# Kernel tuning notes

Measured on AMD Instinct MI355X. Metric: run time of the kernel, lower is better.

The kernel has to match this reference:

```python
import jax, jax.numpy as jnp
import numpy as np

B, T, M, E = 2, 2048, 1024, 8
CAP = (2 * B * T) // E  # GShard top-2 capacity = 2*S/E = 1024


def setup_inputs() -> dict:
    key = jax.random.key(0)
    k1, k2, k3 = jax.random.split(key, 3)
    x = jax.random.normal(k1, (B, T, M), jnp.float32)
    wg = jax.random.normal(k2, (M, E), jnp.float32) * 0.02
    expert_w = jax.random.normal(k3, (E, M, M), jnp.float32) * 0.02
    expert_b = jnp.zeros((E, M), jnp.float32)
    return {"x": x, "wg": wg, "expert_w": expert_w, "expert_b": expert_b}


def _top2_gate(x2, wg, capacity):
    """fairseq/GShard Top2Gate (deterministic second-expert, no jitter).
    Returns (l_aux, combine_weights[S,E,C], dispatch_mask[S,E,C] bool)."""
    S = x2.shape[0]
    num_experts = wg.shape[1]
    logits = x2 @ wg                                  # [S, E]
    gates = jax.nn.softmax(logits, axis=-1)           # [S, E]
    # top-1 expert
    idx1 = jnp.argmax(gates, axis=1)
    mask1 = jax.nn.one_hot(idx1, num_experts, dtype=jnp.int32)
    # top-2 expert: argmax over logits with top-1 masked out
    neg_inf = jnp.finfo(logits.dtype).min
    logits_wo1 = jnp.where(mask1.astype(bool), neg_inf, logits)
    idx2 = jnp.argmax(logits_wo1, axis=1)
    mask2 = jax.nn.one_hot(idx2, num_experts, dtype=jnp.int32)
    # positions within each expert's buffer
    loc1 = jnp.cumsum(mask1, axis=0) - 1              # [S, E]
    loc2 = jnp.cumsum(mask2, axis=0) - 1 + jnp.sum(mask1, axis=0, keepdims=True)
    # load-balancing auxiliary loss
    me = jnp.mean(gates, axis=0)
    ce = jnp.mean(mask1.astype(gates.dtype), axis=0)
    l_aux = jnp.mean(me * ce) * (num_experts * num_experts)
    # drop tokens over capacity
    mask1 = mask1 * (loc1 < capacity).astype(jnp.int32)
    mask2 = mask2 * (loc2 < capacity).astype(jnp.int32)
    loc1_s = jnp.sum(loc1 * mask1, axis=1)            # [S]
    loc2_s = jnp.sum(loc2 * mask2, axis=1)
    m1f = mask1.astype(gates.dtype)
    m2f = mask2.astype(gates.dtype)
    gates1_s = jnp.sum(gates * m1f, axis=1)
    gates2_s = jnp.sum(gates * m2f, axis=1)
    denom = gates1_s + gates2_s
    denom = jnp.clip(denom, jnp.finfo(gates.dtype).eps, None)
    gates1 = gates1_s / denom
    gates2 = gates2_s / denom
    loc1_oh = jax.nn.one_hot(loc1_s, capacity, dtype=gates.dtype)  # [S, C]
    loc2_oh = jax.nn.one_hot(loc2_s, capacity, dtype=gates.dtype)
    combine1 = gates1[:, None, None] * m1f[:, :, None] * loc1_oh[:, None, :]
    combine2 = gates2[:, None, None] * m2f[:, :, None] * loc2_oh[:, None, :]
    combine_weights = combine1 + combine2             # [S, E, C]
    dispatch_mask = combine_weights > 0               # bool [S, E, C]
    return l_aux, combine_weights, dispatch_mask


def reference(x, wg, expert_w, expert_b):
    b, t, d = x.shape
    x2 = x.reshape(-1, d)                             # [S, M]
    l_aux, cw, dm = _top2_gate(x2, wg, CAP)
    dmf = dm.astype(x.dtype)                          # [S, E, C]
    # dispatch: (E*C, S) @ (S, M) -> per-expert token buffers [E, C, M]
    dispatched = jnp.einsum('sec,sm->ecm', dmf, x2)
    # per-expert Linear (single device: all experts local, all-to-all = identity)
    expert_out = jnp.einsum('ecm,emn->ecn', dispatched, expert_w) + expert_b[:, None, :]
    # combine: (S, E*C) @ (E*C, M) -> [S, M]
    combined = jnp.einsum('sec,ecm->sm', cw, expert_out)
    return combined.reshape(b, t, d), l_aux
```

## Files before the change

### kernel.cpp

```cpp
#include <hip/hip_runtime.h>

typedef unsigned short u16;
typedef unsigned int u32;
typedef unsigned long long u64;
typedef short v8s __attribute__((ext_vector_type(8)));
typedef float v4f __attribute__((ext_vector_type(4)));

#define S_TOK 4096
#define MDIM  1024
#define NEXP  8
#define CAPN  1024

__device__ __forceinline__ u16 f2bf(float f) {
  u32 u = __float_as_uint(f);
  u += 0x7FFFu + ((u >> 16) & 1u);
  return (u16)(u >> 16);
}
__device__ __forceinline__ float bf2f(u16 h) {
  return __uint_as_float(((u32)h) << 16);
}
__device__ __forceinline__ void gll16(const void* g, void* l) {
  __builtin_amdgcn_global_load_lds(
      (const __attribute__((address_space(1))) void*)g,
      (__attribute__((address_space(3))) void*)l, 16, 0, 0);
}

__global__ __launch_bounds__(256) void transw_kernel(const float* __restrict__ w,
                                                     u16* __restrict__ wT) {
  int b  = blockIdx.x;
  int e  = b >> 8;
  int mt = (b >> 4) & 15;
  int nt = b & 15;
  __shared__ float tile[64][65];
  const float* src = w + (size_t)e * MDIM * MDIM;
  u16* dst = wT + (size_t)e * MDIM * MDIM;
  int tid = threadIdx.x;
#pragma unroll
  for (int i = 0; i < 16; i++) {
    int idx = tid + i * 256;
    int r = idx >> 6, c = idx & 63;
    tile[r][c] = src[(size_t)(mt * 64 + r) * MDIM + nt * 64 + c];
  }
  __syncthreads();
#pragma unroll
  for (int i = 0; i < 16; i++) {
    int idx = tid + i * 256;
    int r = idx >> 6, c = idx & 63;
    dst[(size_t)(nt * 64 + r) * MDIM + mt * 64 + c] = f2bf(tile[c][r]);
  }
}

__global__ __launch_bounds__(256) void gate_kernel(const float* __restrict__ x,
                                                   const float* __restrict__ wg,
                                                   u16* __restrict__ xbf,
                                                   int4* __restrict__ grec,
                                                   float* __restrict__ gpart) {
  __shared__ float wls[NEXP * MDIM];
  __shared__ float gsh[4][NEXP];
  int tid = threadIdx.x;
  for (int i = tid; i < NEXP * MDIM; i += 256) {
    int m = i >> 3, e = i & 7;
    wls[e * MDIM + m] = wg[i];
  }
  __syncthreads();
  int wave = tid >> 6, lane = tid & 63;
  int s = blockIdx.x * 4 + wave;
  const float* xr = x + (size_t)s * MDIM;
  u16* xw = xbf + (size_t)s * MDIM;
  float acc[NEXP];
#pragma unroll
  for (int e = 0; e < NEXP; e++) acc[e] = 0.f;
#pragma unroll
  for (int j = 0; j < 16; j++) {
    int m = j * 64 + lane;
    float xv = xr[m];
    xw[m] = f2bf(xv);
#pragma unroll
    for (int e = 0; e < NEXP; e++) acc[e] = fmaf(xv, wls[e * MDIM + m], acc[e]);
  }
#pragma unroll
  for (int off = 32; off > 0; off >>= 1)
#pragma unroll
    for (int e = 0; e < NEXP; e++) acc[e] += __shfl_xor(acc[e], off, 64);

  if (lane == 0) {
    float mx = acc[0];
#pragma unroll
    for (int e = 1; e < NEXP; e++) mx = fmaxf(mx, acc[e]);
    float ex[NEXP], sum = 0.f;
#pragma unroll
    for (int e = 0; e < NEXP; e++) { ex[e] = expf(acc[e] - mx); sum += ex[e]; }
    float inv = 1.f / sum;
    int e1 = 0; float b1 = acc[0];
#pragma unroll
    for (int e = 1; e < NEXP; e++) if (acc[e] > b1) { b1 = acc[e]; e1 = e; }
    int e2 = -1; float b2 = -3.4e38f;
#pragma unroll
    for (int e = 0; e < NEXP; e++) if (e != e1 && acc[e] > b2) { b2 = acc[e]; e2 = e; }
    grec[s] = make_int4(e1, e2, __float_as_int(ex[e1] * inv), __float_as_int(ex[e2] * inv));
#pragma unroll
    for (int e = 0; e < NEXP; e++) gsh[wave][e] = ex[e] * inv;
  }
  __syncthreads();
  if (tid < NEXP)
    gpart[blockIdx.x * NEXP + tid] = gsh[0][tid] + gsh[1][tid] + gsh[2][tid] + gsh[3][tid];
}

__global__ __launch_bounds__(1024) void scan_kernel(const int4* __restrict__ grec,
                                                    int4* __restrict__ trec,
                                                    int* __restrict__ slot_token,
                                                    const float* __restrict__ gpart,
                                                    u16* __restrict__ zrow,
                                                    float* __restrict__ out) {
  __shared__ u64 wtot[16][4];
  __shared__ float gred[16][NEXP];
  int t = threadIdx.x, lane = t & 63, wave = t >> 6;

#pragma unroll
  for (int i = 0; i < 8; i++) slot_token[t + i * 1024] = -1;
  zrow[t] = 0;

  float4 p0 = ((const float4*)gpart)[t * 2];
  float4 p1 = ((const float4*)gpart)[t * 2 + 1];
  float gs[NEXP] = {p0.x, p0.y, p0.z, p0.w, p1.x, p1.y, p1.z, p1.w};
#pragma unroll
  for (int off = 32; off > 0; off >>= 1)
#pragma unroll
    for (int e = 0; e < NEXP; e++) gs[e] += __shfl_xor(gs[e], off, 64);
  if (lane == 0)
#pragma unroll
    for (int e = 0; e < NEXP; e++) gred[wave][e] = gs[e];

  int4 r[4];
#pragma unroll
  for (int i = 0; i < 4; i++) r[i] = grec[t * 4 + i];

  u64 a1 = 0, b1 = 0, a2 = 0, b2 = 0;
#pragma unroll
  for (int i = 0; i < 4; i++) {
    int x1 = r[i].x, x2 = r[i].y;
    if (x1 < 4) a1 += 1ULL << (x1 * 16); else b1 += 1ULL << ((x1 - 4) * 16);
    if (x2 < 4) a2 += 1ULL << (x2 * 16); else b2 += 1ULL << ((x2 - 4) * 16);
  }
  u64 ia1 = a1, ib1 = b1, ia2 = a2, ib2 = b2;
#pragma unroll
  for (int off = 1; off < 64; off <<= 1) {
    u64 s1 = __shfl_up(a1, off, 64), s2 = __shfl_up(b1, off, 64);
    u64 s3 = __shfl_up(a2, off, 64), s4 = __shfl_up(b2, off, 64);
    if (lane >= off) { a1 += s1; b1 += s2; a2 += s3; b2 += s4; }
  }
  if (lane == 63) { wtot[wave][0] = a1; wtot[wave][1] = b1; wtot[wave][2] = a2; wtot[wave][3] = b2; }
  __syncthreads();
  if (t < 16) {
    u64 v0 = wtot[t][0], v1 = wtot[t][1], v2 = wtot[t][2], v3 = wtot[t][3];
#pragma unroll
    for (int off = 1; off < 16; off <<= 1) {
      u64 s0 = __shfl_up(v0, off, 64), s1 = __shfl_up(v1, off, 64);
      u64 s2 = __shfl_up(v2, off, 64), s3 = __shfl_up(v3, off, 64);
      if (t >= off) { v0 += s0; v1 += s1; v2 += s2; v3 += s3; }
    }
    wtot[t][0] = v0; wtot[t][1] = v1; wtot[t][2] = v2; wtot[t][3] = v3;
  }
  __syncthreads();
  u64 o1 = 0, o2 = 0, o3 = 0, o4 = 0;
  if (wave > 0) { o1 = wtot[wave - 1][0]; o2 = wtot[wave - 1][1]; o3 = wtot[wave - 1][2]; o4 = wtot[wave - 1][3]; }
  u64 ea  = a1 + o1 - ia1;
  u64 eb  = b1 + o2 - ib1;
  u64 ea2 = a2 + o3 - ia2;
  u64 eb2 = b2 + o4 - ib2;
  u64 ta = wtot[15][0], tb = wtot[15][1];

  int base1[NEXP], base2[NEXP], cnt1[NEXP];
#pragma unroll
  for (int e = 0; e < 4; e++) {
    base1[e]     = (int)((ea  >> (e * 16)) & 0xFFFF);
    base1[4 + e] = (int)((eb  >> (e * 16)) & 0xFFFF);
    base2[e]     = (int)((ea2 >> (e * 16)) & 0xFFFF);
    base2[4 + e] = (int)((eb2 >> (e * 16)) & 0xFFFF);
    cnt1[e]      = (int)((ta  >> (e * 16)) & 0xFFFF);
    cnt1[4 + e]  = (int)((tb  >> (e * 16)) & 0xFFFF);
  }
#pragma unroll
  for (int i = 0; i < 4; i++) {
    int s = t * 4 + i;
    int e1 = r[i].x, e2 = r[i].y;
    float g1 = __int_as_float(r[i].z), g2 = __int_as_float(r[i].w);
    int l1 = 0, l2 = 0;
#pragma unroll
    for (int q = 0; q < NEXP; q++) {
      if (q == e1) { l1 = base1[q]; base1[q] = l1 + 1; }
      if (q == e2) { l2 = base2[q]; base2[q] = l2 + 1; }
    }
    int loc2 = l2 + cnt1[e2];
    bool k1 = l1 < CAPN;
    bool k2 = loc2 < CAPN;
    float g1s = k1 ? g1 : 0.f;
    float g2s = k2 ? g2 : 0.f;
    float denom = fmaxf(g1s + g2s, 1.1920929e-7f);
    float gn1 = g1s / denom, gn2 = g2s / denom;
    int slot1 = k1 ? e1 * CAPN + l1 : -1;
    int slot2 = k2 ? e2 * CAPN + loc2 : -1;
    trec[s] = make_int4(slot1, slot2, __float_as_int(gn1), __float_as_int(gn2));
    if (k1) slot_token[slot1] = s;
    if (k2) slot_token[slot2] = s;
  }
  if (t == 0) {
    float acc = 0.f;
#pragma unroll
    for (int e = 0; e < NEXP; e++) {
      float g = 0.f;
      for (int w = 0; w < 16; w++) g += gred[w][e];
      acc += g * (float)cnt1[e];
    }
    out[(size_t)S_TOK * MDIM] = 8.f * acc / (4096.f * 4096.f);
  }
}

__global__ __launch_bounds__(256, 2) void expert_gemm(const u16* __restrict__ xbf,
                                                      const u16* __restrict__ wT,
                                                      const int* __restrict__ slot_token,
                                                      const u16* __restrict__ zrow,
                                                      const float* __restrict__ bias,
                                                      u16* __restrict__ eoutb) {
  __shared__ __align__(16) u16 As[128 * 64];
  __shared__ __align__(16) u16 Bs[128 * 64];
  const int tid  = threadIdx.x;
  const int e    = blockIdx.x >> 6;
  const int tile = blockIdx.x & 63;
  const int tm   = (tile >> 3) << 7;
  const int tn   = (tile & 7) << 7;
  const int lane = tid & 63;
  const int wave = tid >> 6;
  const int wr = wave >> 1, wc = wave & 1;

  const u16* srcA[4];
  const u16* srcB[4];
#pragma unroll
  for (int it = 0; it < 4; ++it) {
    int off = tid * 16 + it * 4096;
    int row = off >> 7;
    int kb  = off & 127;
    int st  = slot_token[e * CAPN + tm + row];
    srcA[it] = (st >= 0 ? xbf + (size_t)st * MDIM : zrow) + (kb >> 1);
    srcB[it] = wT + (size_t)e * MDIM * MDIM + (size_t)(tn + row) * MDIM + (kb >> 1);
  }
  char* ldsA = (char*)As;
  char* ldsB = (char*)Bs;

  v4f acc[4][4];
#pragma unroll
  for (int i = 0; i < 4; i++)
#pragma unroll
    for (int j = 0; j < 4; j++) acc[i][j] = (v4f){0.f, 0.f, 0.f, 0.f};

  for (int k0 = 0; k0 < MDIM; k0 += 64) {
    __syncthreads();
#pragma unroll
    for (int it = 0; it < 4; ++it)
      gll16(srcA[it] + k0, ldsA + tid * 16 + it * 4096);
#pragma unroll
    for (int it = 0; it < 4; ++it)
      gll16(srcB[it] + k0, ldsB + tid * 16 + it * 4096);
    __syncthreads();

    const v8s* Ap = (const v8s*)As;
    const v8s* Bp = (const v8s*)Bs;
#pragma unroll
    for (int ks = 0; ks < 2; ++ks) {
      v8s af[4], bfr[4];
#pragma unroll
      for (int i = 0; i < 4; i++)
        af[i] = Ap[(wr * 64 + i * 16 + (lane & 15)) * 8 + ks * 4 + (lane >> 4)];
#pragma unroll
      for (int j = 0; j < 4; j++)
        bfr[j] = Bp[(wc * 64 + j * 16 + (lane & 15)) * 8 + ks * 4 + (lane >> 4)];
#pragma unroll
      for (int i = 0; i < 4; i++)
#pragma unroll
        for (int j = 0; j < 4; j++)
          acc[i][j] = __builtin_amdgcn_mfma_f32_16x16x32_bf16(af[i], bfr[j], acc[i][j], 0, 0, 0);
    }
  }

  const float* bp = bias + (size_t)e * MDIM;
  float bv[4];
#pragma unroll
  for (int j = 0; j < 4; j++) bv[j] = bp[tn + wc * 64 + j * 16 + (lane & 15)];
  u16* outp = eoutb + (size_t)e * CAPN * MDIM;
#pragma unroll
  for (int i = 0; i < 4; i++) {
#pragma unroll
    for (int rr = 0; rr < 4; rr++) {
      int row = tm + wr * 64 + i * 16 + (lane >> 4) * 4 + rr;
#pragma unroll
      for (int j = 0; j < 4; j++) {
        int col = tn + wc * 64 + j * 16 + (lane & 15);
        outp[(size_t)row * MDIM + col] = f2bf(acc[i][j][rr] + bv[j]);
      }
    }
  }
}

__global__ __launch_bounds__(256) void combine_kernel(const u16* __restrict__ eoutb,
                                                      const int4* __restrict__ trec,
                                                      float* __restrict__ out) {
  int s = blockIdx.x;
  int tid = threadIdx.x;
  int4 r = trec[s];
  float g1 = __int_as_float(r.z), g2 = __int_as_float(r.w);
  float4 res = make_float4(0.f, 0.f, 0.f, 0.f);
  if (r.x >= 0) {
    ushort4 o = ((const ushort4*)(eoutb + (size_t)r.x * MDIM))[tid];
    res.x += g1 * bf2f(o.x); res.y += g1 * bf2f(o.y);
    res.z += g1 * bf2f(o.z); res.w += g1 * bf2f(o.w);
  }
  if (r.y >= 0) {
    ushort4 o = ((const ushort4*)(eoutb + (size_t)r.y * MDIM))[tid];
    res.x += g2 * bf2f(o.x); res.y += g2 * bf2f(o.y);
    res.z += g2 * bf2f(o.z); res.w += g2 * bf2f(o.w);
  }
  ((float4*)out)[(size_t)s * 256 + tid] = res;
}

extern "C" void kernel_launch(void* const* d_in, const int* in_sizes, int n_in,
                              void* d_out, int out_size, void* d_ws, size_t ws_size,
                              hipStream_t stream) {
  (void)in_sizes; (void)n_in; (void)out_size; (void)ws_size;
  const float* x  = (const float*)d_in[0];
  const float* wg = (const float*)d_in[1];
  const float* ew = (const float*)d_in[2];
  const float* eb = (const float*)d_in[3];
  float* out = (float*)d_out;

  char* ws = (char*)d_ws;
  u16*   xbf   = (u16*)(ws + 0);
  u16*   wT    = (u16*)(ws + 8388608);
  u16*   eoutb = (u16*)(ws + 25165824);
  u16*   zrow  = (u16*)(ws + 41943040);
  int4*  grec  = (int4*)(ws + 41945088);
  int4*  trec  = (int4*)(ws + 42010624);
  int*   slot  = (int*)(ws + 42076160);
  float* gpart = (float*)(ws + 42108928);

  transw_kernel<<<2048, 256, 0, stream>>>(ew, wT);
  gate_kernel<<<1024, 256, 0, stream>>>(x, wg, xbf, grec, gpart);
  scan_kernel<<<1, 1024, 0, stream>>>(grec, trec, slot, gpart, zrow, out);
  expert_gemm<<<512, 256, 0, stream>>>(xbf, wT, slot, zrow, eb, eoutb);
  combine_kernel<<<4096, 256, 0, stream>>>(eoutb, trec, out);
}
```

Before: 147.8 us.

## Merge gate and weight-transpose kernels, fragment-major LDS layout for expert GEMM

Folds the weight transpose/bf16 conversion and the gating kernel into one launch that uses the block index to pick the path, removing a launch and letting the two independent jobs run side by side. The expert GEMM's global-to-LDS loads are remapped so each 16-byte chunk lands in MFMA fragment order, so each lane reads its A/B fragments contiguously (index * 64 + lane) and LDS bank conflicts on fragment reads go away. The merged kernel uses the larger shared-memory footprint for every block, which may lower occupancy on the transpose path, and the remapped global loads are less contiguous per wave.

```diff
diff --git a/kernel.cpp b/kernel.cpp
--- a/kernel.cpp
+++ b/kernel.cpp
@@ -25,85 +25,87 @@
       (__attribute__((address_space(3))) void*)l, 16, 0, 0);
 }
 
-__global__ __launch_bounds__(256) void transw_kernel(const float* __restrict__ w,
-                                                     u16* __restrict__ wT) {
-  int b  = blockIdx.x;
-  int e  = b >> 8;
-  int mt = (b >> 4) & 15;
-  int nt = b & 15;
-  __shared__ float tile[64][65];
-  const float* src = w + (size_t)e * MDIM * MDIM;
-  u16* dst = wT + (size_t)e * MDIM * MDIM;
-  int tid = threadIdx.x;
-#pragma unroll
-  for (int i = 0; i < 16; i++) {
-    int idx = tid + i * 256;
-    int r = idx >> 6, c = idx & 63;
-    tile[r][c] = src[(size_t)(mt * 64 + r) * MDIM + nt * 64 + c];
-  }
-  __syncthreads();
-#pragma unroll
-  for (int i = 0; i < 16; i++) {
-    int idx = tid + i * 256;
-    int r = idx >> 6, c = idx & 63;
-    dst[(size_t)(nt * 64 + r) * MDIM + mt * 64 + c] = f2bf(tile[c][r]);
-  }
-}
-
-__global__ __launch_bounds__(256) void gate_kernel(const float* __restrict__ x,
+__global__ __launch_bounds__(256) void prep_kernel(const float* __restrict__ x,
                                                    const float* __restrict__ wg,
+                                                   const float* __restrict__ w,
                                                    u16* __restrict__ xbf,
+                                                   u16* __restrict__ wT,
                                                    int4* __restrict__ grec,
                                                    float* __restrict__ gpart) {
-  __shared__ float wls[NEXP * MDIM];
-  __shared__ float gsh[4][NEXP];
+  __shared__ float smem[8224];
   int tid = threadIdx.x;
-  for (int i = tid; i < NEXP * MDIM; i += 256) {
-    int m = i >> 3, e = i & 7;
-    wls[e * MDIM + m] = wg[i];
-  }
-  __syncthreads();
-  int wave = tid >> 6, lane = tid & 63;
-  int s = blockIdx.x * 4 + wave;
-  const float* xr = x + (size_t)s * MDIM;
-  u16* xw = xbf + (size_t)s * MDIM;
-  float acc[NEXP];
-#pragma unroll
-  for (int e = 0; e < NEXP; e++) acc[e] = 0.f;
-#pragma unroll
-  for (int j = 0; j < 16; j++) {
-    int m = j * 64 + lane;
-    float xv = xr[m];
-    xw[m] = f2bf(xv);
-#pragma unroll
-    for (int e = 0; e < NEXP; e++) acc[e] = fmaf(xv, wls[e * MDIM + m], acc[e]);
-  }
-#pragma unroll
-  for (int off = 32; off > 0; off >>= 1)
-#pragma unroll
-    for (int e = 0; e < NEXP; e++) acc[e] += __shfl_xor(acc[e], off, 64);
-
-  if (lane == 0) {
-    float mx = acc[0];
-#pragma unroll
-    for (int e = 1; e < NEXP; e++) mx = fmaxf(mx, acc[e]);
-    float ex[NEXP], sum = 0.f;
-#pragma unroll
-    for (int e = 0; e < NEXP; e++) { ex[e] = expf(acc[e] - mx); sum += ex[e]; }
-    float inv = 1.f / sum;
-    int e1 = 0; float b1 = acc[0];
-#pragma unroll
-    for (int e = 1; e < NEXP; e++) if (acc[e] > b1) { b1 = acc[e]; e1 = e; }
-    int e2 = -1; float b2 = -3.4e38f;
-#pragma unroll
-    for (int e = 0; e < NEXP; e++) if (e != e1 && acc[e] > b2) { b2 = acc[e]; e2 = e; }
-    grec[s] = make_int4(e1, e2, __float_as_int(ex[e1] * inv), __float_as_int(ex[e2] * inv));
-#pragma unroll
-    for (int e = 0; e < NEXP; e++) gsh[wave][e] = ex[e] * inv;
-  }
-  __syncthreads();
-  if (tid < NEXP)
-    gpart[blockIdx.x * NEXP + tid] = gsh[0][tid] + gsh[1][tid] + gsh[2][tid] + gsh[3][tid];
+  int b = blockIdx.x;
+  if (b < 1024) {
+    float* wls = smem;
+    float (*gsh)[NEXP] = (float (*)[NEXP])(smem + 8192);
+    for (int i = tid; i < NEXP * MDIM; i += 256) {
+      int m = i >> 3, e = i & 7;
+      wls[e * MDIM + m] = wg[i];
+    }
+    __syncthreads();
+    int wave = tid >> 6, lane = tid & 63;
+    int s = b * 4 + wave;
+    const float* xr = x + (size_t)s * MDIM;
+    u16* xw = xbf + (size_t)s * MDIM;
+    float acc[NEXP];
+#pragma unroll
+    for (int e = 0; e < NEXP; e++) acc[e] = 0.f;
+#pragma unroll
+    for (int j = 0; j < 16; j++) {
+      int m = j * 64 + lane;
+      float xv = xr[m];
+      xw[m] = f2bf(xv);
+#pragma unroll
+      for (int e = 0; e < NEXP; e++) acc[e] = fmaf(xv, wls[e * MDIM + m], acc[e]);
+    }
+#pragma unroll
+    for (int off = 32; off > 0; off >>= 1)
+#pragma unroll
+      for (int e = 0; e < NEXP; e++) acc[e] += __shfl_xor(acc[e], off, 64);
+
+    if (lane == 0) {
+      float mx = acc[0];
+#pragma unroll
+      for (int e = 1; e < NEXP; e++) mx = fmaxf(mx, acc[e]);
+      float ex[NEXP], sum = 0.f;
+#pragma unroll
+      for (int e = 0; e < NEXP; e++) { ex[e] = expf(acc[e] - mx); sum += ex[e]; }
+      float inv = 1.f / sum;
+      int e1 = 0; float b1 = acc[0];
+#pragma unroll
+      for (int e = 1; e < NEXP; e++) if (acc[e] > b1) { b1 = acc[e]; e1 = e; }
+      int e2 = -1; float b2 = -3.4e38f;
+#pragma unroll
+      for (int e = 0; e < NEXP; e++) if (e != e1 && acc[e] > b2) { b2 = acc[e]; e2 = e; }
+      grec[s] = make_int4(e1, e2, __float_as_int(ex[e1] * inv), __float_as_int(ex[e2] * inv));
+#pragma unroll
+      for (int e = 0; e < NEXP; e++) gsh[wave][e] = ex[e] * inv;
+    }
+    __syncthreads();
+    if (tid < NEXP)
+      gpart[b * NEXP + tid] = gsh[0][tid] + gsh[1][tid] + gsh[2][tid] + gsh[3][tid];
+  } else {
+    int bb = b - 1024;
+    int e  = bb >> 8;
+    int mt = (bb >> 4) & 15;
+    int nt = bb & 15;
+    float (*tile)[65] = (float (*)[65])smem;
+    const float* src = w + (size_t)e * MDIM * MDIM;
+    u16* dst = wT + (size_t)e * MDIM * MDIM;
+#pragma unroll
+    for (int i = 0; i < 16; i++) {
+      int idx = tid + i * 256;
+      int r = idx >> 6, c = idx & 63;
+      tile[r][c] = src[(size_t)(mt * 64 + r) * MDIM + nt * 64 + c];
+    }
+    __syncthreads();
+#pragma unroll
+    for (int i = 0; i < 16; i++) {
+      int idx = tid + i * 256;
+      int r = idx >> 6, c = idx & 63;
+      dst[(size_t)(nt * 64 + r) * MDIM + mt * 64 + c] = f2bf(tile[c][r]);
+    }
+  }
 }
 
 __global__ __launch_bounds__(1024) void scan_kernel(const int4* __restrict__ grec,
@@ -209,7 +211,7 @@
 #pragma unroll
     for (int e = 0; e < NEXP; e++) {
       float g = 0.f;
-      for (int w = 0; w < 16; w++) g += gred[w][e];
+      for (int w2 = 0; w2 < 16; w2++) g += gred[w2][e];
       acc += g * (float)cnt1[e];
     }
     out[(size_t)S_TOK * MDIM] = 8.f * acc / (4096.f * 4096.f);
@@ -237,12 +239,12 @@
   const u16* srcB[4];
 #pragma unroll
   for (int it = 0; it < 4; ++it) {
-    int off = tid * 16 + it * 4096;
-    int row = off >> 7;
-    int kb  = off & 127;
-    int st  = slot_token[e * CAPN + tm + row];
-    srcA[it] = (st >= 0 ? xbf + (size_t)st * MDIM : zrow) + (kb >> 1);
-    srcB[it] = wT + (size_t)e * MDIM * MDIM + (size_t)(tn + row) * MDIM + (kb >> 1);
+    int g     = it * 4 + wave;
+    int m_loc = (g >> 1) * 16 + (lane & 15);
+    int kc    = (g & 1) * 4 + (lane >> 4);
+    int st    = slot_token[e * CAPN + tm + m_loc];
+    srcA[it] = (st >= 0 ? xbf + (size_t)st * MDIM : zrow) + kc * 8;
+    srcB[it] = wT + (size_t)e * MDIM * MDIM + (size_t)(tn + m_loc) * MDIM + kc * 8;
   }
   char* ldsA = (char*)As;
   char* ldsB = (char*)Bs;
@@ -270,10 +272,10 @@
       v8s af[4], bfr[4];
 #pragma unroll
       for (int i = 0; i < 4; i++)
-        af[i] = Ap[(wr * 64 + i * 16 + (lane & 15)) * 8 + ks * 4 + (lane >> 4)];
+        af[i] = Ap[((wr * 4 + i) * 2 + ks) * 64 + lane];
 #pragma unroll
       for (int j = 0; j < 4; j++)
-        bfr[j] = Bp[(wc * 64 + j * 16 + (lane & 15)) * 8 + ks * 4 + (lane >> 4)];
+        bfr[j] = Bp[((wc * 4 + j) * 2 + ks) * 64 + lane];
 #pragma unroll
       for (int i = 0; i < 4; i++)
 #pragma unroll
@@ -342,8 +344,7 @@
   int*   slot  = (int*)(ws + 42076160);
   float* gpart = (float*)(ws + 42108928);
 
-  transw_kernel<<<2048, 256, 0, stream>>>(ew, wT);
-  gate_kernel<<<1024, 256, 0, stream>>>(x, wg, xbf, grec, gpart);
+  prep_kernel<<<3072, 256, 0, stream>>>(x, wg, ew, xbf, wT, grec, gpart);
   scan_kernel<<<1, 1024, 0, stream>>>(grec, trec, slot, gpart, zrow, out);
   expert_gemm<<<512, 256, 0, stream>>>(xbf, wT, slot, zrow, eb, eoutb);
   combine_kernel<<<4096, 256, 0, stream>>>(eoutb, trec, out);
```

Result: no change. 150.6 us (+1.9%).
